# Kernel tuning notes

Hardware: AMD Instinct MI355X
Metric: run time of the kernel (lower is better)

The kernel has to match this reference:

```python
import jax, jax.numpy as jnp
import numpy as np

D = 8388608  # vector_dim
N = 1024     # phase table size
M = 1024     # magnitude table size


def setup_inputs() -> dict:
    key = jax.random.key(0)
    k1, k2, k3, k4 = jax.random.split(key, 4)
    ctx_phase_idx = jax.random.randint(k1, (D,), 0, N, dtype=jnp.int64)
    ctx_mag_idx = jax.random.randint(k2, (D,), 0, M, dtype=jnp.int64)
    self_phase_idx = jax.random.randint(k3, (D,), 0, N, dtype=jnp.int64)
    self_mag_idx = jax.random.randint(k4, (D,), 0, M, dtype=jnp.int64)
    # Lookup tables (the ExtendedLookupTableModule's precomputed tables):
    # phase table = cos(2*pi*i/N), its grad = -sin(2*pi*i/N) * (2*pi/N)
    # magnitude table = exp(linspace), its grad = same exp * slope
    phase_grid = 2.0 * jnp.pi * jnp.arange(N, dtype=jnp.float32) / N
    mag_grid = jnp.linspace(-1.0, 1.0, M, dtype=jnp.float32)
    cos_table = jnp.cos(phase_grid)
    cos_grad_table = -jnp.sin(phase_grid) * (2.0 * jnp.pi / N)
    exp_table = jnp.exp(mag_grid)
    exp_grad_table = exp_table * (2.0 / (M - 1))
    return {
        "ctx_phase_idx": ctx_phase_idx,
        "ctx_mag_idx": ctx_mag_idx,
        "self_phase_idx": self_phase_idx,
        "self_mag_idx": self_mag_idx,
        "cos_table": cos_table,
        "exp_table": exp_table,
        "cos_grad_table": cos_grad_table,
        "exp_grad_table": exp_grad_table,
    }


def reference(ctx_phase_idx, ctx_mag_idx, self_phase_idx, self_mag_idx,
              cos_table, exp_table, cos_grad_table, exp_grad_table):
    # mod-indexed sums
    phase_out = (ctx_phase_idx + self_phase_idx) % N  # [D] int
    mag_out = (ctx_mag_idx + self_mag_idx) % M        # [D] int
    # four table gathers
    cos_vals = cos_table[phase_out]       # [D]
    exp_vals = exp_table[mag_out]         # [D]
    dcos = cos_grad_table[phase_out]      # [D]
    dexp = exp_grad_table[mag_out]        # [D]
    # elementwise multiplies + reduction
    signal = cos_vals * exp_vals          # [D]
    grad_phase = dcos * exp_vals          # [D]
    grad_mag = cos_vals * dexp            # [D]
    strength = signal.sum()
    return (phase_out, mag_out, signal, strength, grad_phase, grad_mag)
```

## Files before the change

### kernel.cpp

```cpp
#include <hip/hip_runtime.h>

constexpr int D_TOTAL = 8388608;
constexpr int TBL = 1024;
constexpr int IDX_MASK = 1023;
constexpr int BLOCK = 256;
constexpr int VEC = 8;
constexpr int ELEMS_PER_BLOCK = BLOCK * VEC;
constexpr int NBLOCKS = D_TOTAL / ELEMS_PER_BLOCK;

typedef float f32x4 __attribute__((ext_vector_type(4)));
typedef float f32x8 __attribute__((ext_vector_type(8)));
typedef int   i32x8 __attribute__((ext_vector_type(8)));
typedef f32x4 f32x4u __attribute__((aligned(4)));

__global__ __launch_bounds__(BLOCK) void phasecell_main(
    const int* __restrict__ ctx_p, const int* __restrict__ ctx_m,
    const int* __restrict__ self_p, const int* __restrict__ self_m,
    const float* __restrict__ cos_t, const float* __restrict__ exp_t,
    const float* __restrict__ dcos_t, const float* __restrict__ dexp_t,
    float* __restrict__ out, float* __restrict__ block_sums) {
  __shared__ float2 s_phase[TBL];
  __shared__ float2 s_mag[TBL];
  for (int i = threadIdx.x; i < TBL; i += BLOCK) {
    s_phase[i] = make_float2(cos_t[i], dcos_t[i]);
    s_mag[i]   = make_float2(exp_t[i], dexp_t[i]);
  }
  __syncthreads();

  const int base = (blockIdx.x * BLOCK + threadIdx.x) * VEC;

  const i32x8 cp = *reinterpret_cast<const i32x8*>(ctx_p + base);
  const i32x8 cm = *reinterpret_cast<const i32x8*>(ctx_m + base);
  const i32x8 sp = *reinterpret_cast<const i32x8*>(self_p + base);
  const i32x8 sm = *reinterpret_cast<const i32x8*>(self_m + base);

  int p[VEC], m[VEC];
#pragma unroll
  for (int j = 0; j < VEC; ++j) {
    p[j] = (cp[j] + sp[j]) & IDX_MASK;
    m[j] = (cm[j] + sm[j]) & IDX_MASK;
  }

  f32x8 po, mo, sig;
  f32x4 gph0, gph1, gmg0, gmg1;
  float local = 0.f;
#pragma unroll
  for (int j = 0; j < VEC; ++j) {
    const float2 ph = s_phase[p[j]];
    const float2 mg = s_mag[m[j]];
    const float s = ph.x * mg.x;
    sig[j] = s;
    const float gp = ph.y * mg.x;
    const float gm = ph.x * mg.y;
    if (j < 4) { gph0[j] = gp; gmg0[j] = gm; }
    else       { gph1[j - 4] = gp; gmg1[j - 4] = gm; }
    po[j] = (float)p[j];
    mo[j] = (float)m[j];
    local += s;
  }

  *reinterpret_cast<f32x8*>(out + base)                = po;
  *reinterpret_cast<f32x8*>(out + D_TOTAL + base)      = mo;
  *reinterpret_cast<f32x8*>(out + 2 * D_TOTAL + base)  = sig;

  float* gp_base = out + 3 * D_TOTAL + 1 + base;
  float* gm_base = out + 4 * D_TOTAL + 1 + base;
  *reinterpret_cast<f32x4u*>(gp_base)     = gph0;
  *reinterpret_cast<f32x4u*>(gp_base + 4) = gph1;
  *reinterpret_cast<f32x4u*>(gm_base)     = gmg0;
  *reinterpret_cast<f32x4u*>(gm_base + 4) = gmg1;

#pragma unroll
  for (int off = 32; off > 0; off >>= 1) local += __shfl_down(local, off, 64);
  __shared__ float wsum[BLOCK / 64];
  const int wave = threadIdx.x >> 6;
  const int lane = threadIdx.x & 63;
  if (lane == 0) wsum[wave] = local;
  __syncthreads();
  if (threadIdx.x == 0) {
    float t = 0.f;
#pragma unroll
    for (int w = 0; w < BLOCK / 64; ++w) t += wsum[w];
    block_sums[blockIdx.x] = t;
  }
}

__global__ __launch_bounds__(BLOCK) void phasecell_reduce(
    const float* __restrict__ partials, float* __restrict__ strength_out) {
  float s = 0.f;
  for (int i = threadIdx.x; i < NBLOCKS; i += BLOCK) s += partials[i];
#pragma unroll
  for (int off = 32; off > 0; off >>= 1) s += __shfl_down(s, off, 64);
  __shared__ float wsum[BLOCK / 64];
  const int wave = threadIdx.x >> 6;
  const int lane = threadIdx.x & 63;
  if (lane == 0) wsum[wave] = s;
  __syncthreads();
  if (threadIdx.x == 0) {
    float t = 0.f;
#pragma unroll
    for (int w = 0; w < BLOCK / 64; ++w) t += wsum[w];
    strength_out[0] = t;
  }
}

extern "C" void kernel_launch(void* const* d_in, const int* in_sizes, int n_in,
                              void* d_out, int out_size, void* d_ws, size_t ws_size,
                              hipStream_t stream) {
  const int* ctx_p  = (const int*)d_in[0];
  const int* ctx_m  = (const int*)d_in[1];
  const int* self_p = (const int*)d_in[2];
  const int* self_m = (const int*)d_in[3];
  const float* cos_t  = (const float*)d_in[4];
  const float* exp_t  = (const float*)d_in[5];
  const float* dcos_t = (const float*)d_in[6];
  const float* dexp_t = (const float*)d_in[7];
  float* out = (float*)d_out;
  float* block_sums = (float*)d_ws;

  phasecell_main<<<NBLOCKS, BLOCK, 0, stream>>>(
      ctx_p, ctx_m, self_p, self_m, cos_t, exp_t, dcos_t, dexp_t, out, block_sums);
  phasecell_reduce<<<1, BLOCK, 0, stream>>>(block_sums, out + 3 * (size_t)D_TOTAL);
}
```

Before: 290.5 us.

## Realign shifted gradient stores via neighbor exchange and use nontemporal stores

The gradient outputs sit at an offset of one float, so the old code issued unaligned 4-wide stores. The new code shifts each thread's values by one element, taking the previous element from its neighbor through shared memory or by recomputing it at block edges. This lets every gradient store be an aligned 8-wide write. All output stores also become nontemporal to reduce cache pollution. The cost is an extra barrier, a shared-memory exchange and a few scalar global loads per block.

```diff
diff --git a/kernel.cpp b/kernel.cpp
--- a/kernel.cpp
+++ b/kernel.cpp
@@ -8,10 +8,8 @@
 constexpr int ELEMS_PER_BLOCK = BLOCK * VEC;
 constexpr int NBLOCKS = D_TOTAL / ELEMS_PER_BLOCK;
 
-typedef float f32x4 __attribute__((ext_vector_type(4)));
 typedef float f32x8 __attribute__((ext_vector_type(8)));
 typedef int   i32x8 __attribute__((ext_vector_type(8)));
-typedef f32x4 f32x4u __attribute__((aligned(4)));
 
 __global__ __launch_bounds__(BLOCK) void phasecell_main(
     const int* __restrict__ ctx_p, const int* __restrict__ ctx_m,
@@ -21,13 +19,14 @@
     float* __restrict__ out, float* __restrict__ block_sums) {
   __shared__ float2 s_phase[TBL];
   __shared__ float2 s_mag[TBL];
-  for (int i = threadIdx.x; i < TBL; i += BLOCK) {
+  const int tid = threadIdx.x;
+  for (int i = tid; i < TBL; i += BLOCK) {
     s_phase[i] = make_float2(cos_t[i], dcos_t[i]);
     s_mag[i]   = make_float2(exp_t[i], dexp_t[i]);
   }
   __syncthreads();
 
-  const int base = (blockIdx.x * BLOCK + threadIdx.x) * VEC;
+  const int base = (blockIdx.x * BLOCK + tid) * VEC;
 
   const i32x8 cp = *reinterpret_cast<const i32x8*>(ctx_p + base);
   const i32x8 cm = *reinterpret_cast<const i32x8*>(ctx_m + base);
@@ -42,7 +41,7 @@
   }
 
   f32x8 po, mo, sig;
-  f32x4 gph0, gph1, gmg0, gmg1;
+  float gph[VEC], gmg[VEC];
   float local = 0.f;
 #pragma unroll
   for (int j = 0; j < VEC; ++j) {
@@ -50,34 +49,62 @@
     const float2 mg = s_mag[m[j]];
     const float s = ph.x * mg.x;
     sig[j] = s;
-    const float gp = ph.y * mg.x;
-    const float gm = ph.x * mg.y;
-    if (j < 4) { gph0[j] = gp; gmg0[j] = gm; }
-    else       { gph1[j - 4] = gp; gmg1[j - 4] = gm; }
+    gph[j] = ph.y * mg.x;
+    gmg[j] = ph.x * mg.y;
     po[j] = (float)p[j];
     mo[j] = (float)m[j];
     local += s;
   }
 
-  *reinterpret_cast<f32x8*>(out + base)                = po;
-  *reinterpret_cast<f32x8*>(out + D_TOTAL + base)      = mo;
-  *reinterpret_cast<f32x8*>(out + 2 * D_TOTAL + base)  = sig;
+  __builtin_nontemporal_store(po,  (f32x8*)(out + base));
+  __builtin_nontemporal_store(mo,  (f32x8*)(out + D_TOTAL + base));
+  __builtin_nontemporal_store(sig, (f32x8*)(out + 2 * D_TOTAL + base));
 
-  float* gp_base = out + 3 * D_TOTAL + 1 + base;
-  float* gm_base = out + 4 * D_TOTAL + 1 + base;
-  *reinterpret_cast<f32x4u*>(gp_base)     = gph0;
-  *reinterpret_cast<f32x4u*>(gp_base + 4) = gph1;
-  *reinterpret_cast<f32x4u*>(gm_base)     = gmg0;
-  *reinterpret_cast<f32x4u*>(gm_base + 4) = gmg1;
+  __shared__ float2 s_lastg[BLOCK];
+  s_lastg[tid] = make_float2(gph[VEC - 1], gmg[VEC - 1]);
+  __syncthreads();
+
+  float pgp, pgm;
+  if (tid > 0) {
+    const float2 t = s_lastg[tid - 1];
+    pgp = t.x;
+    pgm = t.y;
+  } else if (blockIdx.x > 0) {
+    const int e = blockIdx.x * ELEMS_PER_BLOCK - 1;
+    const int pp = (ctx_p[e] + self_p[e]) & IDX_MASK;
+    const int mm = (ctx_m[e] + self_m[e]) & IDX_MASK;
+    pgp = s_phase[pp].y * s_mag[mm].x;
+    pgm = s_phase[pp].x * s_mag[mm].y;
+  } else {
+    const int e = D_TOTAL - 1;
+    const int pp = (ctx_p[e] + self_p[e]) & IDX_MASK;
+    const int mm = (ctx_m[e] + self_m[e]) & IDX_MASK;
+    const float gpL = s_phase[pp].y * s_mag[mm].x;
+    const float gmL = s_phase[pp].x * s_mag[mm].y;
+    pgp = 0.0f;
+    pgm = gpL;
+    out[5 * (size_t)D_TOTAL] = gmL;
+  }
+
+  f32x8 wph, wmg;
+  wph[0] = pgp;
+  wmg[0] = pgm;
+#pragma unroll
+  for (int k = 1; k < VEC; ++k) {
+    wph[k] = gph[k - 1];
+    wmg[k] = gmg[k - 1];
+  }
+  __builtin_nontemporal_store(wph, (f32x8*)(out + 3 * D_TOTAL + base));
+  __builtin_nontemporal_store(wmg, (f32x8*)(out + 4 * D_TOTAL + base));
 
 #pragma unroll
   for (int off = 32; off > 0; off >>= 1) local += __shfl_down(local, off, 64);
   __shared__ float wsum[BLOCK / 64];
-  const int wave = threadIdx.x >> 6;
-  const int lane = threadIdx.x & 63;
+  const int wave = tid >> 6;
+  const int lane = tid & 63;
   if (lane == 0) wsum[wave] = local;
   __syncthreads();
-  if (threadIdx.x == 0) {
+  if (tid == 0) {
     float t = 0.f;
 #pragma unroll
     for (int w = 0; w < BLOCK / 64; ++w) t += wsum[w];
```

Measured after the change: 323.1 us. 11.3% more time.
